# Kernel optimization log

Hardware: AMD Instinct MI355X
Metric: run time of the kernel (lower is better)

The kernel has to match this reference:

```python
import jax, jax.numpy as jnp
import numpy as np

BN_EPS = 1e-5
L2_EPS = 1e-12

def _conv2d(x, w, pad):
    # x: NCHW, w: OIHW
    return jax.lax.conv_general_dilated(
        x, w, window_strides=(1, 1), padding=[(pad, pad), (pad, pad)],
        dimension_numbers=('NCHW', 'OIHW', 'NCHW'))

def _l2norm(x, axis):
    n = jnp.sqrt(jnp.sum(x * x, axis=axis, keepdims=True))
    return x / jnp.maximum(n, L2_EPS)

def setup_inputs() -> dict:
    key = jax.random.key(0)
    ks = jax.random.split(key, 8)
    x = jax.random.normal(ks[0], (16, 512, 32, 32), dtype=jnp.float32)
    w_proj1 = jax.random.normal(ks[1], (512, 512, 3, 3), dtype=jnp.float32) * 0.02
    bn_gamma = jnp.ones((512,), dtype=jnp.float32)
    bn_beta = jnp.zeros((512,), dtype=jnp.float32)
    bn_mean = jnp.zeros((512,), dtype=jnp.float32)
    bn_var = jnp.ones((512,), dtype=jnp.float32)
    w_proj2 = jax.random.normal(ks[2], (512, 512, 3, 3), dtype=jnp.float32) * 0.02
    w_assign = jax.random.normal(ks[3], (64, 512, 1, 1), dtype=jnp.float32)
    centroids = jax.random.uniform(ks[4], (64, 512), dtype=jnp.float32)
    return {'x': x, 'w_proj1': w_proj1, 'bn_gamma': bn_gamma, 'bn_beta': bn_beta,
            'bn_mean': bn_mean, 'bn_var': bn_var, 'w_proj2': w_proj2,
            'w_assign': w_assign, 'centroids': centroids}

def reference(x, w_proj1, bn_gamma, bn_beta, bn_mean, bn_var, w_proj2, w_assign, centroids):
    # projection head: conv3x3 -> BN (eval) -> ReLU -> conv3x3
    h = _conv2d(x, w_proj1, pad=1)
    inv = jax.lax.rsqrt(bn_var + BN_EPS)
    h = (h - bn_mean[None, :, None, None]) * (bn_gamma * inv)[None, :, None, None] + bn_beta[None, :, None, None]
    h = jax.nn.relu(h)
    x_enc = _conv2d(h, w_proj2, pad=1)

    # descriptor-wise L2 normalization over channels
    xn = _l2norm(x_enc, axis=1)
    N, C, H, W = xn.shape
    K = w_assign.shape[0]

    # soft assignment: 1x1 conv -> softmax over clusters
    sa = _conv2d(xn, w_assign, pad=0).reshape(N, K, H * W)  # [N,K,L]
    sa = jax.nn.softmax(sa, axis=1)

    xf = xn.reshape(N, C, H * W)  # [N,C,L]
    # algebraic rewrite of the per-cluster residual loop:
    # vlad[n,k,c] = sum_l sa[n,k,l]*(xf[n,c,l] - cent[k,c])
    vlad = jnp.einsum('nkl,ncl->nkc', sa, xf) - sa.sum(-1)[:, :, None] * centroids[None]
    vlad = _l2norm(vlad, axis=2)          # intra-normalization
    vlad = vlad.reshape(N, K * C)
    vlad = _l2norm(vlad, axis=1)          # global L2 norm
    return (vlad, x_enc)
```

## Files before the change

### kernel.cpp

```cpp
#include <hip/hip_runtime.h>
#include <math.h>


typedef __bf16 bf16x8 __attribute__((ext_vector_type(8)));
typedef float f32x4 __attribute__((ext_vector_type(4)));

#define GLDS16(gp, lp)                                                  \
  __builtin_amdgcn_global_load_lds(                                     \
      (const __attribute__((address_space(1))) void*)(gp),              \
      (__attribute__((address_space(3))) void*)(lp), 16, 0, 0)

template <int MODE>
__global__ __launch_bounds__(256) void conv_gemm(
    const __bf16* __restrict__ in,
    const __bf16* __restrict__ wt,
    const float* __restrict__ scale, const float* __restrict__ shift,
    __bf16* __restrict__ outp) {
  __shared__ __align__(16) __bf16 Hl[6 * 42 * 64];
  __shared__ __align__(16) __bf16 Wl[2 * 128 * 64];

  const int t = threadIdx.x;
  const int bx = blockIdx.x, oT = blockIdx.y;
  const int lane = t & 63, wid = t >> 6;
  const int l16 = lane & 15, q = lane >> 4;
  const int wrow = wid >> 1, wcol = wid & 1;

  const int n = bx >> 3;
  const int trow0 = (bx & 7) * 4;

  const int swr = t >> 3, sp = t & 7;
  const __bf16* wsrc[4];
#pragma unroll
  for (int i = 0; i < 4; ++i)
    wsrc[i] = wt + (size_t)(oT * 128 + 32 * i + swr) * 4608 + sp * 8;

  const __bf16* inb = in + (size_t)n * (1156 * 512);
  const __bf16* hsrc[8];
  bool hval[8];
#pragma unroll
  for (int i = 0; i < 8; ++i) {
    const int jj = t + 256 * i;
    hval[i] = jj < 2016;
    const int hr = jj / 336;
    const int hrem = jj - hr * 336;
    const int hw = hrem >> 3, hc8 = hrem & 7;
    hsrc[i] = inb + ((size_t)((trow0 + hr) * 34 + hw)) * 512 +
              (hc8 ^ (hw & 7)) * 8;
  }

  const int c0 = (q ^ (l16 & 7)) * 8;
  const int c1 = ((4 + q) ^ (l16 & 7)) * 8;
  int aoff[4], prow_[4], pcol_[4];
#pragma unroll
  for (int i = 0; i < 4; ++i) {
    aoff[i] = (wrow * 64 + i * 16 + l16) * 64;
    const int p = wcol * 64 + i * 16 + l16;
    prow_[i] = p >> 5;
    pcol_[i] = p & 31;
  }

  f32x4 acc[4][4];
#pragma unroll
  for (int i = 0; i < 4; ++i)
#pragma unroll
    for (int j = 0; j < 4; ++j) acc[i][j] = (f32x4){0.f, 0.f, 0.f, 0.f};

#pragma unroll
  for (int i = 0; i < 8; ++i)
    if (hval[i]) GLDS16(hsrc[i], Hl + (t + 256 * i) * 8);
#pragma unroll
  for (int i = 0; i < 4; ++i)
    GLDS16(wsrc[i], Wl + (t + 256 * i) * 8);
#pragma unroll
  for (int i = 0; i < 4; ++i)
    GLDS16(wsrc[i] + 512, Wl + 8192 + (t + 256 * i) * 8);
  asm volatile("s_waitcnt vmcnt(4)" ::: "memory");
  __builtin_amdgcn_s_barrier();

  int tap = 0, dh = 0, dw = 0, cc = 0;
  int tap2 = 2, cc2 = 0;

#pragma unroll 1
  for (int s = 0; s < 72; ++s) {
    const int buf = (s & 1) << 13;
    const __bf16* Wb = Wl + buf;

    bf16x8 aw[4][2], bp[4][2];
#pragma unroll
    for (int i = 0; i < 4; ++i) {
      aw[i][0] = *(const bf16x8*)&Wb[aoff[i] + c0];
      aw[i][1] = *(const bf16x8*)&Wb[aoff[i] + c1];
    }
#pragma unroll
    for (int i = 0; i < 4; ++i) {
      const int col = pcol_[i] + dw;
      const int rb = (prow_[i] + dh) * 2688 + col * 64;
      const int xr = col & 7;
      bp[i][0] = *(const bf16x8*)&Hl[rb + (q ^ xr) * 8];
      bp[i][1] = *(const bf16x8*)&Hl[rb + ((4 + q) ^ xr) * 8];
    }
    asm volatile("s_waitcnt lgkmcnt(0)" ::: "memory");
    __builtin_amdgcn_sched_barrier(0);
    __builtin_amdgcn_s_barrier();

    if (tap == 8 && cc < 7) {
#pragma unroll
      for (int i = 0; i < 8; ++i)
        if (hval[i]) GLDS16(hsrc[i] + (cc + 1) * 64, Hl + (t + 256 * i) * 8);
    }
    if (s < 70) {
      const int woffs2 = (tap2 * 8 + cc2) * 64;
#pragma unroll
      for (int i = 0; i < 4; ++i)
        GLDS16(wsrc[i] + woffs2, Wl + buf + (t + 256 * i) * 8);
    }

    __builtin_amdgcn_s_setprio(1);
#pragma unroll
    for (int kh = 0; kh < 2; ++kh)
#pragma unroll
      for (int mt = 0; mt < 4; ++mt)
#pragma unroll
        for (int nt = 0; nt < 4; ++nt)
          acc[mt][nt] = __builtin_amdgcn_mfma_f32_16x16x32_bf16(
              aw[mt][kh], bp[nt][kh], acc[mt][nt], 0, 0, 0);
    __builtin_amdgcn_s_setprio(0);

    if (s < 70)
      asm volatile("s_waitcnt vmcnt(4)" ::: "memory");
    else
      asm volatile("s_waitcnt vmcnt(0)" ::: "memory");
    __builtin_amdgcn_s_barrier();

    ++tap;
    ++dw;
    if (dw == 3) {
      dw = 0;
      ++dh;
    }
    if (tap == 9) {
      tap = 0;
      dh = 0;
      dw = 0;
      ++cc;
    }
    if (++tap2 == 9) {
      tap2 = 0;
      ++cc2;
    }
  }

#pragma unroll
  for (int nt = 0; nt < 4; ++nt) {
    const int m_l = wcol * 64 + nt * 16 + l16;
    const int mg2 = bx * 128 + m_l;
    const int n2 = mg2 >> 10, pix2 = mg2 & 1023;
#pragma unroll
    for (int mt = 0; mt < 4; ++mt) {
      const int ob = oT * 128 + wrow * 64 + mt * 16 + q * 4;
      f32x4 v = acc[mt][nt];
      union {
        __bf16 b[4];
        uint2 u;
      } pk;
      if (MODE == 0) {
        const f32x4 sc = *(const f32x4*)&scale[ob];
        const f32x4 sh = *(const f32x4*)&shift[ob];
#pragma unroll
        for (int r = 0; r < 4; ++r)
          pk.b[r] = (__bf16)fmaxf(v[r] * sc[r] + sh[r], 0.f);
        __bf16* dst = outp +
                      ((size_t)n2 * 1156 + ((pix2 >> 5) + 1) * 34 +
                       ((pix2 & 31) + 1)) * 512 + ob;
        *(uint2*)dst = pk.u;
      } else {
#pragma unroll
        for (int r = 0; r < 4; ++r) pk.b[r] = (__bf16)v[r];
        __bf16* dst = outp + ((size_t)n2 * 1024 + pix2) * 512 + ob;
        *(uint2*)dst = pk.u;
      }
    }
  }
}

__global__ __launch_bounds__(256) void xform(const float* __restrict__ x,
                                             __bf16* __restrict__ xpad) {
  const int n = blockIdx.x >> 5, h = blockIdx.x & 31;
  const int t = threadIdx.x;
  const int w = t & 31, cg = t >> 5;
  const float* src = x + ((size_t)n * 512 + cg * 64) * 1024 + h * 32 + w;
  __bf16* dst =
      xpad + ((size_t)n * 1156 + (h + 1) * 34 + (w + 1)) * 512 + cg * 64;
  union {
    __bf16 b[8];
    uint4 u;
  } pk;
#pragma unroll 1
  for (int jj = 0; jj < 8; ++jj) {
#pragma unroll
    for (int j = 0; j < 8; ++j) pk.b[j] = (__bf16)src[(jj * 8 + j) * 1024];
    *(uint4*)(dst + jj * 8) = pk.u;
  }
}

__global__ __launch_bounds__(256) void expand_x(const __bf16* __restrict__ xebT,
                                                float* __restrict__ xenc,
                                                __bf16* __restrict__ xeb) {
  __shared__ __align__(16) __bf16 Ll[64 * 64];
  const int t = threadIdx.x;
  const int cc = blockIdx.x, ptile = blockIdx.y, n = blockIdx.z;
  const int p0 = ptile * 64, c0 = cc * 64;
#pragma unroll
  for (int i = 0; i < 2; ++i) {
    const int u = t * 2 + i;
    const int pix = u >> 3, c8 = u & 7;
    uint4 v =
        *(const uint4*)&xebT[((size_t)n * 1024 + p0 + pix) * 512 + c0 + c8 * 8];
    *(uint4*)&Ll[pix * 64 + (c8 ^ (pix & 7)) * 8] = v;
  }
  __syncthreads();
  const int c = t >> 2, g = t & 3;
  union {
    float f[4];
    float4 v;
  } fv[4];
  union {
    __bf16 b[16];
    uint4 u[2];
  } bv;
#pragma unroll
  for (int r = 0; r < 16; ++r) {
    const int pix = g * 16 + r;
    __bf16 b = Ll[pix * 64 + ((c >> 3) ^ (pix & 7)) * 8 + (c & 7)];
    bv.b[r] = b;
    fv[r >> 2].f[r & 3] = (float)b;
  }
  float* fd = xenc + ((size_t)n * 512 + c0 + c) * 1024 + p0 + g * 16;
#pragma unroll
  for (int r = 0; r < 4; ++r) *(float4*)(fd + r * 4) = fv[r].v;
  __bf16* bd = xeb + ((size_t)n * 512 + c0 + c) * 1024 + p0 + g * 16;
  *(uint4*)bd = bv.u[0];
  *(uint4*)(bd + 8) = bv.u[1];
}

__global__ __launch_bounds__(256) void assign_softmax(
    const __bf16* __restrict__ xebT, const __bf16* __restrict__ watb,
    __bf16* __restrict__ saPb, float* __restrict__ S) {
  __shared__ __align__(16) __bf16 Al[64 * 32];
  __shared__ __align__(16) __bf16 Wlb[64 * 32];
  __shared__ float Sl[64];
  const int t = threadIdx.x;
  const int pt = blockIdx.x, n = blockIdx.y;
  const int lane = t & 63, wid = t >> 6;
  const int l16 = lane & 15, q = lane >> 4;
  if (t < 64) Sl[t] = 0.f;

  const int arow = t >> 2;
  const __bf16* asrc = xebT + ((size_t)n * 1024 + pt * 64 + arow) * 512 +
                       ((t & 3) ^ ((arow >> 1) & 3)) * 8;
  const __bf16* wsrc = watb + (size_t)(t >> 2) * 512 + (t & 3) * 8;
  const int ldsb = wid * 512;
  const int sw = (q ^ ((l16 >> 1) & 3)) * 8;
  const int pnoff = (t >> 2) * 32 + (t & 3) * 8;

  f32x4 acc[4];
#pragma unroll
  for (int i = 0; i < 4; ++i) acc[i] = (f32x4){0.f, 0.f, 0.f, 0.f};
  float pn = 0.f;

#pragma unroll 1
  for (int kc = 0; kc < 16; ++kc) {
    GLDS16(asrc + kc * 32, Al + ldsb);
    GLDS16(wsrc + kc * 32, Wlb + ldsb);
    __syncthreads();
    {
      bf16x8 v = *(const bf16x8*)&Al[pnoff];
#pragma unroll
      for (int j = 0; j < 8; ++j) {
        float f = (float)v[j];
        pn = fmaf(f, f, pn);
      }
    }
    bf16x8 pf = *(const bf16x8*)&Al[(wid * 16 + l16) * 32 + sw];
    bf16x8 wf[4];
#pragma unroll
    for (int ka = 0; ka < 4; ++ka)
      wf[ka] = *(const bf16x8*)&Wlb[(ka * 16 + l16) * 32 + sw];
#pragma unroll
    for (int ka = 0; ka < 4; ++ka)
      acc[ka] =
          __builtin_amdgcn_mfma_f32_16x16x32_bf16(wf[ka], pf, acc[ka], 0, 0, 0);
    __syncthreads();
  }
  pn += __shfl_xor(pn, 1);
  pn += __shfl_xor(pn, 2);
  const float rn = 1.0f / fmaxf(sqrtf(__shfl(pn, l16 * 4)), 1e-12f);

  float sc[16];
  float m = -3.4e38f;
#pragma unroll
  for (int ka = 0; ka < 4; ++ka)
#pragma unroll
    for (int r = 0; r < 4; ++r) {
      float v = acc[ka][r] * rn;
      sc[ka * 4 + r] = v;
      m = fmaxf(m, v);
    }
  m = fmaxf(m, __shfl_xor(m, 16));
  m = fmaxf(m, __shfl_xor(m, 32));
  float s = 0.f;
#pragma unroll
  for (int j = 0; j < 16; ++j) {
    sc[j] = __expf(sc[j] - m);
    s += sc[j];
  }
  s += __shfl_xor(s, 16);
  s += __shfl_xor(s, 32);
  const float inv = 1.0f / s;
  const int pixg = pt * 64 + wid * 16 + l16;
#pragma unroll
  for (int j = 0; j < 16; ++j) {
    const int k = (j >> 2) * 16 + q * 4 + (j & 3);
    float sa = sc[j] * inv;
    sc[j] = sa;
    saPb[((size_t)n * 64 + k) * 1024 + pixg] = (__bf16)(sa * rn);
  }
#pragma unroll
  for (int j = 0; j < 16; ++j) {
    float v = sc[j];
    v += __shfl_xor(v, 1);
    v += __shfl_xor(v, 2);
    v += __shfl_xor(v, 4);
    v += __shfl_xor(v, 8);
    sc[j] = v;
  }
  if (l16 == 0) {
#pragma unroll
    for (int j = 0; j < 16; ++j)
      atomicAdd(&Sl[(j >> 2) * 16 + q * 4 + (j & 3)], sc[j]);
  }
  __syncthreads();
  if (t < 64) atomicAdd(&S[n * 64 + t], Sl[t]);
}

__global__ __launch_bounds__(256) void vlad_gemm(
    const __bf16* __restrict__ saPb, const __bf16* __restrict__ xeb,
    float* __restrict__ vpart) {
  __shared__ __align__(16) __bf16 Al[64 * 32];
  __shared__ __align__(16) __bf16 Bl[128 * 32];

  const int t = threadIdx.x;
  const int cT = blockIdx.x, n = blockIdx.y, ks = blockIdx.z;
  const int lane = t & 63, wid = t >> 6;
  const int l16 = lane & 15, q = lane >> 4;
  const int wrow = wid >> 1, wcol = wid & 1;

  const int ar = t >> 2, acp = t & 3;
  const __bf16* asrc = saPb + (size_t)n * 65536 + (size_t)ar * 1024 + ks * 256 +
                       (acp ^ ((ar >> 1) & 3)) * 8;
  const int br0 = t >> 2, bcp0 = t & 3;
  const int br1 = (t + 256) >> 2, bcp1 = t & 3;
  const __bf16* bsrc0 = xeb + (size_t)n * 524288 +
                        (size_t)(cT * 128 + br0) * 1024 + ks * 256 +
                        (bcp0 ^ ((br0 >> 1) & 3)) * 8;
  const __bf16* bsrc1 = xeb + (size_t)n * 524288 +
                        (size_t)(cT * 128 + br1) * 1024 + ks * 256 +
                        (bcp1 ^ ((br1 >> 1) & 3)) * 8;

  const int ldsb = wid * 512;
  const int sw = (q ^ ((l16 >> 1) & 3)) * 8;

  f32x4 acc[2][4];
#pragma unroll
  for (int i = 0; i < 2; ++i)
#pragma unroll
    for (int j = 0; j < 4; ++j) acc[i][j] = (f32x4){0.f, 0.f, 0.f, 0.f};

#pragma unroll 1
  for (int kc = 0; kc < 8; ++kc) {
    GLDS16(asrc + kc * 32, Al + ldsb);
    GLDS16(bsrc0 + kc * 32, Bl + ldsb);
    GLDS16(bsrc1 + kc * 32, Bl + 2048 + ldsb);
    __syncthreads();

    bf16x8 af[2], bf[4];
#pragma unroll
    for (int i = 0; i < 2; ++i)
      af[i] = *(const bf16x8*)&Al[(wrow * 32 + i * 16 + l16) * 32 + sw];
#pragma unroll
    for (int i = 0; i < 4; ++i)
      bf[i] = *(const bf16x8*)&Bl[(wcol * 64 + i * 16 + l16) * 32 + sw];
#pragma unroll
    for (int mt = 0; mt < 2; ++mt)
#pragma unroll
      for (int nt = 0; nt < 4; ++nt)
        acc[mt][nt] = __builtin_amdgcn_mfma_f32_16x16x32_bf16(
            af[mt], bf[nt], acc[mt][nt], 0, 0, 0);
    __syncthreads();
  }

  float* vp = vpart + (size_t)(ks * 16 + n) * 32768;
#pragma unroll
  for (int mt = 0; mt < 2; ++mt) {
    const int krow = wrow * 32 + mt * 16 + q * 4;
#pragma unroll
    for (int nt = 0; nt < 4; ++nt) {
      const int ccol = cT * 128 + wcol * 64 + nt * 16 + l16;
#pragma unroll
      for (int r = 0; r < 4; ++r)
        vp[(size_t)(krow + r) * 512 + ccol] = acc[mt][nt][r];
    }
  }
}

__global__ __launch_bounds__(64) void intra_norm(float* __restrict__ vraw,
                                                 const float* __restrict__ vpart,
                                                 const float* __restrict__ S,
                                                 const float* __restrict__ cent,
                                                 float* __restrict__ gss) {
  const int b = blockIdx.x;
  const int n = b >> 6, k = b & 63;
  const int lane = threadIdx.x;
  const float s = S[b];
  float v[8];
  float ss = 0.f;
#pragma unroll
  for (int j = 0; j < 8; ++j) {
    const int c = lane * 8 + j;
    const size_t off = (size_t)b * 512 + c;
    float val = vpart[off] + vpart[524288 + off] + vpart[2 * 524288 + off] +
                vpart[3 * 524288 + off] - s * cent[k * 512 + c];
    v[j] = val;
    ss += val * val;
  }
#pragma unroll
  for (int off = 1; off < 64; off <<= 1) ss += __shfl_xor(ss, off);
  const float rn = 1.0f / fmaxf(sqrtf(ss), 1e-12f);
#pragma unroll
  for (int j = 0; j < 8; ++j) vraw[(size_t)b * 512 + lane * 8 + j] = v[j] * rn;
  if (lane == 0) atomicAdd(&gss[n], ss * rn * rn);
}

__global__ __launch_bounds__(256) void finalize(const float* __restrict__ vraw,
                                                const float* __restrict__ gss,
                                                float* __restrict__ out) {
  const int id = blockIdx.x * 256 + threadIdx.x;
  const int n = id >> 15;
  out[id] = vraw[id] * (1.0f / fmaxf(sqrtf(gss[n]), 1e-12f));
}

__global__ __launch_bounds__(256) void zero_border(__bf16* __restrict__ xpad,
                                                   __bf16* __restrict__ hpad) {
  const int id = blockIdx.x * 256 + threadIdx.x;
  const int n = id / 8448;
  const int rem = id - n * 8448;
  const int pb = rem >> 6;
  const int c8 = rem & 63;
  int h, w;
  if (pb < 34) {
    h = 0;
    w = pb;
  } else if (pb < 68) {
    h = 33;
    w = pb - 34;
  } else {
    const int r2 = pb - 68;
    h = 1 + (r2 >> 1);
    w = (r2 & 1) * 33;
  }
  __bf16* base = blockIdx.y ? hpad : xpad;
  *(uint4*)(base + ((size_t)n * 1156 + h * 34 + w) * 512 + c8 * 8) =
      (uint4){0u, 0u, 0u, 0u};
}

__global__ __launch_bounds__(256) void wt_prep(const float* __restrict__ w1,
                                               const float* __restrict__ w2,
                                               __bf16* __restrict__ wt1,
                                               __bf16* __restrict__ wt2) {
  __shared__ float Lw[4608];
  const int o = blockIdx.x;
  const float* w = blockIdx.y ? w2 : w1;
  __bf16* wt = blockIdx.y ? wt2 : wt1;
  const int t = threadIdx.x;
#pragma unroll
  for (int i = 0; i < 18; ++i)
    Lw[t + 256 * i] = w[(size_t)o * 4608 + t + 256 * i];
  __syncthreads();
#pragma unroll
  for (int i = 0; i < 18; ++i) {
    const int idk = t + 256 * i;
    const int kt = idk >> 6;
    const int p = (idk >> 3) & 7, e = idk & 7;
    const int logical = p ^ (o & 7);
    const int k2 = kt * 64 + logical * 8 + e;
    const int tap = k2 >> 9, ci = k2 & 511;
    wt[(size_t)o * 4608 + idk] = (__bf16)Lw[ci * 9 + tap];
  }
}

__global__ void misc_prep(const float* g, const float* b, const float* m,
                          const float* v, const float* wA, float* scale,
                          float* shift, __bf16* watb, float* Sz) {
  const int i = blockIdx.x * 256 + threadIdx.x;
  if (i < 512) {
    float sc = g[i] / sqrtf(v[i] + 1e-5f);
    scale[i] = sc;
    shift[i] = b[i] - m[i] * sc;
  } else if (i < 512 + 32768) {
    const int id = i - 512;
    const int k = id >> 9, j = id & 511;
    const int kt = j >> 5, cpos = (j >> 3) & 3, e = j & 7;
    const int c = kt * 32 + (cpos ^ ((k >> 1) & 3)) * 8 + e;
    watb[(size_t)k * 512 + j] = (__bf16)wA[(size_t)k * 512 + c];
  } else if (i < 512 + 32768 + 1040) {
    Sz[i - (512 + 32768)] = 0.f;
  }
}

extern "C" void kernel_launch(void* const* d_in, const int* in_sizes, int n_in,
                              void* d_out, int out_size, void* d_ws,
                              size_t ws_size, hipStream_t stream) {
  const float* x = (const float*)d_in[0];
  const float* w1 = (const float*)d_in[1];
  const float* gam = (const float*)d_in[2];
  const float* bet = (const float*)d_in[3];
  const float* mean = (const float*)d_in[4];
  const float* var = (const float*)d_in[5];
  const float* w2 = (const float*)d_in[6];
  const float* wA = (const float*)d_in[7];
  const float* cent = (const float*)d_in[8];
  float* out = (float*)d_out;

  char* ws = (char*)d_ws;
  __bf16* Wt1 = (__bf16*)(ws + 0);
  __bf16* Wt2 = (__bf16*)(ws + 4718592);
  __bf16* xpad = (__bf16*)(ws + 9437184);
  __bf16* xebT = (__bf16*)(ws + 9437184);
  __bf16* saPb = (__bf16*)(ws + 26214400);
  __bf16* hpad = (__bf16*)(ws + 28377088);
  __bf16* xeb = (__bf16*)(ws + 28377088);
  float* vpart = (float*)(ws + 0);
  float* vraw = (float*)(ws + 8388608);
  float* scale = (float*)(ws + 47316992);
  float* shift = (float*)(ws + 47319040);
  __bf16* watb = (__bf16*)(ws + 47321088);
  float* S = (float*)(ws + 47386624);
  float* gss = (float*)(ws + 47390720);

  float* xenc = out + 524288;

  zero_border<<<dim3(528, 2), 256, 0, stream>>>(xpad, hpad);
  misc_prep<<<135, 256, 0, stream>>>(gam, bet, mean, var, wA, scale, shift,
                                     watb, S);
  wt_prep<<<dim3(512, 2), 256, 0, stream>>>(w1, w2, Wt1, Wt2);
  xform<<<512, 256, 0, stream>>>(x, xpad);

  conv_gemm<0><<<dim3(128, 4), 256, 0, stream>>>(xpad, Wt1, scale, shift, hpad);
  conv_gemm<1><<<dim3(128, 4), 256, 0, stream>>>(hpad, Wt2, nullptr, nullptr,
                                                 xebT);

  expand_x<<<dim3(8, 16, 16), 256, 0, stream>>>(xebT, xenc, xeb);
  assign_softmax<<<dim3(16, 16), 256, 0, stream>>>(xebT, watb, saPb, S);
  vlad_gemm<<<dim3(4, 16, 4), 256, 0, stream>>>(saPb, xeb, vpart);
  intra_norm<<<1024, 64, 0, stream>>>(vraw, vpart, S, cent, gss);
  finalize<<<2048, 256, 0, stream>>>(vraw, gss, out);
}
```

Before: 316.0 us.

## Double conv GEMM output-channel tile to 256 and split MFMA around barrier

```diff
diff --git a/kernel.cpp b/kernel.cpp
--- a/kernel.cpp
+++ b/kernel.cpp
@@ -11,13 +11,13 @@
       (__attribute__((address_space(3))) void*)(lp), 16, 0, 0)
 
 template <int MODE>
-__global__ __launch_bounds__(256) void conv_gemm(
+__global__ __launch_bounds__(256, 1) void conv_gemm(
     const __bf16* __restrict__ in,
     const __bf16* __restrict__ wt,
     const float* __restrict__ scale, const float* __restrict__ shift,
     __bf16* __restrict__ outp) {
   __shared__ __align__(16) __bf16 Hl[6 * 42 * 64];
-  __shared__ __align__(16) __bf16 Wl[2 * 128 * 64];
+  __shared__ __align__(16) __bf16 Wl[2 * 256 * 64];
 
   const int t = threadIdx.x;
   const int bx = blockIdx.x, oT = blockIdx.y;
@@ -29,10 +29,10 @@
   const int trow0 = (bx & 7) * 4;
 
   const int swr = t >> 3, sp = t & 7;
-  const __bf16* wsrc[4];
-#pragma unroll
-  for (int i = 0; i < 4; ++i)
-    wsrc[i] = wt + (size_t)(oT * 128 + 32 * i + swr) * 4608 + sp * 8;
+  const __bf16* wsrc[8];
+#pragma unroll
+  for (int i = 0; i < 8; ++i)
+    wsrc[i] = wt + (size_t)(oT * 256 + 32 * i + swr) * 4608 + sp * 8;
 
   const __bf16* inb = in + (size_t)n * (1156 * 512);
   const __bf16* hsrc[8];
@@ -50,18 +50,19 @@
 
   const int c0 = (q ^ (l16 & 7)) * 8;
   const int c1 = ((4 + q) ^ (l16 & 7)) * 8;
-  int aoff[4], prow_[4], pcol_[4];
+  int aoff[8], prow_[4], pcol_[4];
+#pragma unroll
+  for (int i = 0; i < 8; ++i) aoff[i] = (wrow * 128 + i * 16 + l16) * 64;
 #pragma unroll
   for (int i = 0; i < 4; ++i) {
-    aoff[i] = (wrow * 64 + i * 16 + l16) * 64;
     const int p = wcol * 64 + i * 16 + l16;
     prow_[i] = p >> 5;
     pcol_[i] = p & 31;
   }
 
-  f32x4 acc[4][4];
-#pragma unroll
-  for (int i = 0; i < 4; ++i)
+  f32x4 acc[8][4];
+#pragma unroll
+  for (int i = 0; i < 8; ++i)
 #pragma unroll
     for (int j = 0; j < 4; ++j) acc[i][j] = (f32x4){0.f, 0.f, 0.f, 0.f};
 
@@ -69,12 +70,12 @@
   for (int i = 0; i < 8; ++i)
     if (hval[i]) GLDS16(hsrc[i], Hl + (t + 256 * i) * 8);
 #pragma unroll
-  for (int i = 0; i < 4; ++i)
+  for (int i = 0; i < 8; ++i)
     GLDS16(wsrc[i], Wl + (t + 256 * i) * 8);
 #pragma unroll
-  for (int i = 0; i < 4; ++i)
-    GLDS16(wsrc[i] + 512, Wl + 8192 + (t + 256 * i) * 8);
-  asm volatile("s_waitcnt vmcnt(4)" ::: "memory");
+  for (int i = 0; i < 8; ++i)
+    GLDS16(wsrc[i] + 512, Wl + 16384 + (t + 256 * i) * 8);
+  asm volatile("s_waitcnt vmcnt(8)" ::: "memory");
   __builtin_amdgcn_s_barrier();
 
   int tap = 0, dh = 0, dw = 0, cc = 0;
@@ -82,23 +83,35 @@
 
 #pragma unroll 1
   for (int s = 0; s < 72; ++s) {
-    const int buf = (s & 1) << 13;
+    const int buf = (s & 1) << 14;
     const __bf16* Wb = Wl + buf;
 
-    bf16x8 aw[4][2], bp[4][2];
-#pragma unroll
-    for (int i = 0; i < 4; ++i) {
-      aw[i][0] = *(const bf16x8*)&Wb[aoff[i] + c0];
-      aw[i][1] = *(const bf16x8*)&Wb[aoff[i] + c1];
-    }
+    bf16x8 aw0[8], aw1[8], bp0[4], bp1[4];
+    int rbs[4], xrs[4];
+#pragma unroll
+    for (int i = 0; i < 8; ++i) aw0[i] = *(const bf16x8*)&Wb[aoff[i] + c0];
 #pragma unroll
     for (int i = 0; i < 4; ++i) {
       const int col = pcol_[i] + dw;
-      const int rb = (prow_[i] + dh) * 2688 + col * 64;
-      const int xr = col & 7;
-      bp[i][0] = *(const bf16x8*)&Hl[rb + (q ^ xr) * 8];
-      bp[i][1] = *(const bf16x8*)&Hl[rb + ((4 + q) ^ xr) * 8];
-    }
+      rbs[i] = (prow_[i] + dh) * 2688 + col * 64;
+      xrs[i] = col & 7;
+      bp0[i] = *(const bf16x8*)&Hl[rbs[i] + (q ^ xrs[i]) * 8];
+    }
+#pragma unroll
+    for (int i = 0; i < 8; ++i) aw1[i] = *(const bf16x8*)&Wb[aoff[i] + c1];
+#pragma unroll
+    for (int i = 0; i < 4; ++i)
+      bp1[i] = *(const bf16x8*)&Hl[rbs[i] + ((4 + q) ^ xrs[i]) * 8];
+
+    __builtin_amdgcn_s_setprio(1);
+#pragma unroll
+    for (int mt = 0; mt < 8; ++mt)
+#pragma unroll
+      for (int nt = 0; nt < 4; ++nt)
+        acc[mt][nt] = __builtin_amdgcn_mfma_f32_16x16x32_bf16(
+            aw0[mt], bp0[nt], acc[mt][nt], 0, 0, 0);
+    __builtin_amdgcn_s_setprio(0);
+
     asm volatile("s_waitcnt lgkmcnt(0)" ::: "memory");
     __builtin_amdgcn_sched_barrier(0);
     __builtin_amdgcn_s_barrier();
@@ -111,23 +124,21 @@
     if (s < 70) {
       const int woffs2 = (tap2 * 8 + cc2) * 64;
 #pragma unroll
-      for (int i = 0; i < 4; ++i)
+      for (int i = 0; i < 8; ++i)
         GLDS16(wsrc[i] + woffs2, Wl + buf + (t + 256 * i) * 8);
     }
 
     __builtin_amdgcn_s_setprio(1);
 #pragma unroll
-    for (int kh = 0; kh < 2; ++kh)
-#pragma unroll
-      for (int mt = 0; mt < 4; ++mt)
-#pragma unroll
-        for (int nt = 0; nt < 4; ++nt)
-          acc[mt][nt] = __builtin_amdgcn_mfma_f32_16x16x32_bf16(
-              aw[mt][kh], bp[nt][kh], acc[mt][nt], 0, 0, 0);
+    for (int mt = 0; mt < 8; ++mt)
+#pragma unroll
+      for (int nt = 0; nt < 4; ++nt)
+        acc[mt][nt] = __builtin_amdgcn_mfma_f32_16x16x32_bf16(
+            aw1[mt], bp1[nt], acc[mt][nt], 0, 0, 0);
     __builtin_amdgcn_s_setprio(0);
 
     if (s < 70)
-      asm volatile("s_waitcnt vmcnt(4)" ::: "memory");
+      asm volatile("s_waitcnt vmcnt(8)" ::: "memory");
     else
       asm volatile("s_waitcnt vmcnt(0)" ::: "memory");
     __builtin_amdgcn_s_barrier();
@@ -156,8 +167,8 @@
     const int mg2 = bx * 128 + m_l;
     const int n2 = mg2 >> 10, pix2 = mg2 & 1023;
 #pragma unroll
-    for (int mt = 0; mt < 4; ++mt) {
-      const int ob = oT * 128 + wrow * 64 + mt * 16 + q * 4;
+    for (int mt = 0; mt < 8; ++mt) {
+      const int ob = oT * 256 + wrow * 128 + mt * 16 + q * 4;
       f32x4 v = acc[mt][nt];
       union {
         __bf16 b[4];
@@ -555,8 +566,8 @@
   wt_prep<<<dim3(512, 2), 256, 0, stream>>>(w1, w2, Wt1, Wt2);
   xform<<<512, 256, 0, stream>>>(x, xpad);
 
-  conv_gemm<0><<<dim3(128, 4), 256, 0, stream>>>(xpad, Wt1, scale, shift, hpad);
-  conv_gemm<1><<<dim3(128, 4), 256, 0, stream>>>(hpad, Wt2, nullptr, nullptr,
+  conv_gemm<0><<<dim3(128, 2), 256, 0, stream>>>(xpad, Wt1, scale, shift, hpad);
+  conv_gemm<1><<<dim3(128, 2), 256, 0, stream>>>(hpad, Wt2, nullptr, nullptr,
                                                  xebT);
 
   expand_x<<<dim3(8, 16, 16), 256, 0, stream>>>(xebT, xenc, xeb);
```

Result: slower. 403.0 us (+27.6%).
